# Kernel tuning notes

Hardware: AMD Instinct MI355X
Metric: run time of the kernel (lower is better)

Reference implementation:

```python
import jax, jax.numpy as jnp
import numpy as np

IN_F = 4096
OUT_F = 11008
GROUP = 128
BATCH = 32
Q_OUT = OUT_F // 2          # two int4 values packed per byte along out dim
N_GROUPS = IN_F // GROUP    # 32 groups


def setup_inputs() -> dict:
    key = jax.random.key(0)
    k1, k2, k3, k4, k5 = jax.random.split(key, 5)
    inp = jax.random.normal(k1, (BATCH, 1, IN_F), dtype=jnp.float32)
    qweight = jax.random.randint(k2, (IN_F, Q_OUT), 0, 256, dtype=jnp.int32)   # packed bytes
    scales = jax.random.uniform(k3, (N_GROUPS, OUT_F), dtype=jnp.float32) * 0.01
    qzeros = jax.random.randint(k4, (N_GROUPS, Q_OUT), 0, 256, dtype=jnp.int32)  # packed bytes
    bias = jax.random.normal(k5, (OUT_F,), dtype=jnp.float32)
    return {"input": inp, "qweight": qweight, "scales": scales, "qzeros": qzeros, "bias": bias}


def _unpack_int4(packed, n_out):
    # packed: [rows, n_out//2] bytes; low nibble -> even out col, high nibble -> odd out col
    low = packed & 0xF
    high = (packed >> 4) & 0xF
    return jnp.stack([low, high], axis=-1).reshape(packed.shape[0], n_out)


def reference(input, qweight, scales, qzeros, bias):
    # GPTQ-style grouped dequant: w[k, n] = (q[k, n] - zero[g(k), n]) * scale[g(k), n]
    q = _unpack_int4(qweight, OUT_F).astype(jnp.float32)   # [K, N]
    z = _unpack_int4(qzeros, OUT_F).astype(jnp.float32)    # [G, N]
    gidx = jnp.arange(IN_F) // GROUP                       # [K] group index per input channel
    w = (q - z[gidx]) * scales[gidx]                       # [K, N] dequantized weight
    # decode GEMV/GEMM: [B, 1, K] x [K, N] -> [B, 1, N], plus bias (mm_bias_int4 path)
    return jnp.einsum('bsk,kn->bsn', input, w) + bias
```

## Files before the change

kernel.cpp:

```cpp
#include <hip/hip_runtime.h>
#include <hip/hip_fp16.h>
#include <cstdint>

#define IN_F 4096
#define OUT_F 11008
#define Q_OUT 5504
#define GROUP 128
#define BATCH 32

#define KBS 8
#define GPB 4
#define NCH 8
#define BN 64
#define BROWS 66

typedef _Float16 f16x8 __attribute__((ext_vector_type(8)));
typedef float    f32x4 __attribute__((ext_vector_type(4)));

__global__ __launch_bounds__(256)
void xprep_kernel(const float* __restrict__ x, uint4* __restrict__ xf)
{
    const int t    = blockIdx.x * 256 + threadIdx.x;
    const int lane = t & 63;
    const int f    = (t >> 6) & 1;
    const int S    = t >> 7;
    const int m    = f * 16 + (lane & 15);
    const int k0   = S * 32 + (lane >> 4) * 8;
    const float4* xr = reinterpret_cast<const float4*>(x + (size_t)m * IN_F + k0);
    float4 a = xr[0], b = xr[1];
    union { _Float16 h[8]; uint4 u; } v;
    v.h[0] = (_Float16)a.x; v.h[1] = (_Float16)a.y;
    v.h[2] = (_Float16)a.z; v.h[3] = (_Float16)a.w;
    v.h[4] = (_Float16)b.x; v.h[5] = (_Float16)b.y;
    v.h[6] = (_Float16)b.z; v.h[7] = (_Float16)b.w;
    xf[t] = v.u;
}

__global__ __launch_bounds__(256)
void int4_gemm_kernel(const uint4* __restrict__ xf,
                      const int*   __restrict__ qw,
                      const float* __restrict__ scales,
                      const int*   __restrict__ qz,
                      float*       __restrict__ partial)
{
    const int tid  = threadIdx.x;
    const int lane = tid & 63;
    const int wid  = tid >> 6;
    const int nb   = blockIdx.x;
    const int kb   = blockIdx.y;
    const int g0   = kb * GPB;
    const int k0b  = g0 * GROUP;

    __shared__ uint4 a_lds[NCH * 4 * 64];
    __shared__ int   b_lds[2][32 * BROWS];

    const int cl  = lane & 15;
    const int kg  = lane >> 4;
    const int w   = wid * 8 + (cl >> 1);
    const int shn = (cl & 1) * 4;

    const int n = nb * BN + wid * 16 + cl;
    uint    zmu[GPB];
    __half2 spk[GPB];
    #pragma unroll
    for (int g = 0; g < GPB; ++g) {
        const float s = scales[(size_t)(g0 + g) * OUT_F + n];
        const int   z = (qz[(size_t)(g0 + g) * Q_OUT + (n >> 1)] >> shn) & 15;
        spk[g] = __float2half2_rn(s);
        zmu[g] = 0x64006400u + (uint)z * 0x00010001u;
    }

    {
        const size_t gbase = (size_t)(k0b / 32) * 2 * 64;
        #pragma unroll
        for (int r = 0; r < 8; ++r) {
            const uint4* gp = xf + gbase + (size_t)r * 256 + tid;
            __builtin_amdgcn_global_load_lds(
                (const __attribute__((address_space(1))) uint32_t*)gp,
                (__attribute__((address_space(3))) uint32_t*)&a_lds[r * 256 + wid * 64],
                16, 0, 0);
        }
    }

    const int a8 = tid & 7;
    const int bk = tid >> 3;

    f32x4 acc[2] = {};
    uint4 br0[2], br1[2];

    auto LOADB = [&](int c, int set) {
        const int kr = k0b + c * 64;
        br0[set] = *reinterpret_cast<const uint4*>(qw + (size_t)(kr + bk)      * Q_OUT + nb * 32 + a8 * 4);
        br1[set] = *reinterpret_cast<const uint4*>(qw + (size_t)(kr + bk + 32) * Q_OUT + nb * 32 + a8 * 4);
    };
    auto WLDS = [&](int buf, int set) {
        int* p = b_lds[buf];
        p[(4 * a8 + 0) * BROWS + bk]      = br0[set].x;
        p[(4 * a8 + 1) * BROWS + bk]      = br0[set].y;
        p[(4 * a8 + 2) * BROWS + bk]      = br0[set].z;
        p[(4 * a8 + 3) * BROWS + bk]      = br0[set].w;
        p[(4 * a8 + 0) * BROWS + bk + 32] = br1[set].x;
        p[(4 * a8 + 1) * BROWS + bk + 32] = br1[set].y;
        p[(4 * a8 + 2) * BROWS + bk + 32] = br1[set].z;
        p[(4 * a8 + 3) * BROWS + bk + 32] = br1[set].w;
    };

    LOADB(0, 0);
    LOADB(1, 1);
    WLDS(0, 0);
    asm volatile("s_waitcnt vmcnt(0) lgkmcnt(0)" ::: "memory");
    __builtin_amdgcn_s_barrier();
    asm volatile("" ::: "memory");

    #pragma unroll
    for (int c = 0; c < NCH; ++c) {
        const int cur = c & 1;
        if (c + 2 < NCH) LOADB(c + 2, cur);

        const __half2 zmh = __builtin_bit_cast(__half2, zmu[c >> 1]);
        const __half2 sg  = spk[c >> 1];

        #pragma unroll
        for (int s = 0; s < 2; ++s) {
            const int* bp = &b_lds[cur][w * BROWS + s * 32 + kg * 8];
            int2 q0 = *reinterpret_cast<const int2*>(bp + 0);
            int2 q1 = *reinterpret_cast<const int2*>(bp + 2);
            int2 q2 = *reinterpret_cast<const int2*>(bp + 4);
            int2 q3 = *reinterpret_cast<const int2*>(bp + 6);

            union { uint u[4]; f16x8 v; } bf;
            const int2 qq[4] = {q0, q1, q2, q3};
            #pragma unroll
            for (int t = 0; t < 4; ++t) {
                uint pr = __builtin_amdgcn_perm((uint)qq[t].y, (uint)qq[t].x, 0x0C040C00u);
                pr >>= shn;
                uint qk = (pr & 0x000F000Fu) | 0x64006400u;
                __half2 wv = __hmul2(__hsub2(__builtin_bit_cast(__half2, qk), zmh), sg);
                bf.u[t] = __builtin_bit_cast(uint, wv);
            }
            uint4 a0u = a_lds[(c * 4 + s * 2 + 0) * 64 + lane];
            uint4 a1u = a_lds[(c * 4 + s * 2 + 1) * 64 + lane];
            f16x8 af0 = __builtin_bit_cast(f16x8, a0u);
            f16x8 af1 = __builtin_bit_cast(f16x8, a1u);
            acc[0] = __builtin_amdgcn_mfma_f32_16x16x32_f16(af0, bf.v, acc[0], 0, 0, 0);
            acc[1] = __builtin_amdgcn_mfma_f32_16x16x32_f16(af1, bf.v, acc[1], 0, 0, 0);
        }

        if (c + 1 < NCH) {
            WLDS(cur ^ 1, cur ^ 1);
            asm volatile("s_waitcnt lgkmcnt(0)" ::: "memory");
            __builtin_amdgcn_s_barrier();
            asm volatile("" ::: "memory");
        }
    }

    #pragma unroll
    for (int f = 0; f < 2; ++f) {
        const int m = f * 16 + kg * 4;
        float* pp = partial + ((size_t)(kb * BATCH + m)) * OUT_F + n;
        pp[0]                 = acc[f][0];
        pp[(size_t)OUT_F]     = acc[f][1];
        pp[(size_t)OUT_F * 2] = acc[f][2];
        pp[(size_t)OUT_F * 3] = acc[f][3];
    }
}

__global__ __launch_bounds__(256)
void reduce_bias_kernel(const float* __restrict__ partial,
                        const float* __restrict__ bias,
                        float* __restrict__ out)
{
    const int i4 = (blockIdx.x * 256 + threadIdx.x) * 4;
    const int n  = i4 % OUT_F;
    float4 s = *reinterpret_cast<const float4*>(bias + n);
    #pragma unroll
    for (int kb = 0; kb < KBS; ++kb) {
        float4 p = *reinterpret_cast<const float4*>(partial + (size_t)kb * BATCH * OUT_F + i4);
        s.x += p.x; s.y += p.y; s.z += p.z; s.w += p.w;
    }
    *reinterpret_cast<float4*>(out + i4) = s;
}

extern "C" void kernel_launch(void* const* d_in, const int* in_sizes, int n_in,
                              void* d_out, int out_size, void* d_ws, size_t ws_size,
                              hipStream_t stream)
{
    const float* inp    = (const float*)d_in[0];
    const int*   qw     = (const int*)d_in[1];
    const float* scales = (const float*)d_in[2];
    const int*   qz     = (const int*)d_in[3];
    const float* bias   = (const float*)d_in[4];
    float*       out    = (float*)d_out;

    const size_t XFB = (size_t)BATCH * IN_F * 2;
    uint4* xf      = (uint4*)d_ws;
    float* partial = (float*)((char*)d_ws + XFB);

    xprep_kernel<<<64, 256, 0, stream>>>(inp, xf);

    int4_gemm_kernel<<<dim3(OUT_F / BN, KBS), 256, 0, stream>>>(
        xf, qw, scales, qz, partial);

    reduce_bias_kernel<<<(BATCH * OUT_F) / 1024, 256, 0, stream>>>(partial, bias, out);
}
```

Before: 31.46 us.

## Quantize activations to int8 and use i8 MFMA with atomic split-K reduction

Activations are quantized per row to int8 with a max-abs scale, and per-group activation sums are precomputed. The GEMM then runs on i8 MFMA instructions using raw int4 nibbles, and zero-points and scales are applied after accumulation using those sums. The separate reduce kernel is replaced by initializing the output with bias in the prep kernel and accumulating split-K partials with atomic adds. Weight dequantization math and the partial-buffer round trip go away, at the cost of int8 quantization error on activations and nondeterministic float atomics.

```diff
diff --git a/kernel.cpp b/kernel.cpp
--- a/kernel.cpp
+++ b/kernel.cpp
@@ -1,5 +1,4 @@
 #include <hip/hip_runtime.h>
-#include <hip/hip_fp16.h>
 #include <cstdint>
 
 #define IN_F 4096
@@ -12,36 +11,79 @@
 #define GPB 4
 #define NCH 8
 #define BN 64
-#define BROWS 66
-
-typedef _Float16 f16x8 __attribute__((ext_vector_type(8)));
-typedef float    f32x4 __attribute__((ext_vector_type(4)));
+#define BST 18
+
+typedef int   i32x4 __attribute__((ext_vector_type(4)));
+typedef float f32x4 __attribute__((ext_vector_type(4)));
 
 __global__ __launch_bounds__(256)
-void xprep_kernel(const float* __restrict__ x, uint4* __restrict__ xf)
+void prep_kernel(const float* __restrict__ x,
+                 const float* __restrict__ bias,
+                 uint4* __restrict__ xq,
+                 int*   __restrict__ Sx,
+                 float* __restrict__ delta,
+                 float* __restrict__ out)
 {
-    const int t    = blockIdx.x * 256 + threadIdx.x;
-    const int lane = t & 63;
-    const int f    = (t >> 6) & 1;
-    const int S    = t >> 7;
-    const int m    = f * 16 + (lane & 15);
-    const int k0   = S * 32 + (lane >> 4) * 8;
-    const float4* xr = reinterpret_cast<const float4*>(x + (size_t)m * IN_F + k0);
-    float4 a = xr[0], b = xr[1];
-    union { _Float16 h[8]; uint4 u; } v;
-    v.h[0] = (_Float16)a.x; v.h[1] = (_Float16)a.y;
-    v.h[2] = (_Float16)a.z; v.h[3] = (_Float16)a.w;
-    v.h[4] = (_Float16)b.x; v.h[5] = (_Float16)b.y;
-    v.h[6] = (_Float16)b.z; v.h[7] = (_Float16)b.w;
-    xf[t] = v.u;
+    const int t = threadIdx.x;
+    if (blockIdx.x >= 32) {
+        const int j4 = ((blockIdx.x - 32) * 256 + t) * 4;
+        *reinterpret_cast<float4*>(out + j4) =
+            *reinterpret_cast<const float4*>(bias + (j4 % OUT_F));
+        return;
+    }
+    const int m = blockIdx.x;
+    const float* xr = x + (size_t)m * IN_F + t * 16;
+    float4 v[4];
+    #pragma unroll
+    for (int i = 0; i < 4; ++i) v[i] = reinterpret_cast<const float4*>(xr)[i];
+
+    float lm = 0.f;
+    #pragma unroll
+    for (int i = 0; i < 4; ++i) {
+        lm = fmaxf(lm, fmaxf(fmaxf(fabsf(v[i].x), fabsf(v[i].y)),
+                             fmaxf(fabsf(v[i].z), fabsf(v[i].w))));
+    }
+    #pragma unroll
+    for (int d = 32; d; d >>= 1) lm = fmaxf(lm, __shfl_xor(lm, d));
+    __shared__ float wred[4];
+    if ((t & 63) == 0) wred[t >> 6] = lm;
+    __syncthreads();
+    const float mx  = fmaxf(fmaxf(wred[0], wred[1]), fmaxf(wred[2], wred[3]));
+    const float inv = mx > 0.f ? 127.0f / mx : 0.f;
+
+    int q[16];
+    #pragma unroll
+    for (int i = 0; i < 4; ++i) {
+        q[i * 4 + 0] = __float2int_rn(v[i].x * inv);
+        q[i * 4 + 1] = __float2int_rn(v[i].y * inv);
+        q[i * 4 + 2] = __float2int_rn(v[i].z * inv);
+        q[i * 4 + 3] = __float2int_rn(v[i].w * inv);
+    }
+    uint4 w;
+    uint* wp = reinterpret_cast<uint*>(&w);
+    #pragma unroll
+    for (int i = 0; i < 4; ++i)
+        wp[i] = (q[i*4] & 255) | ((q[i*4+1] & 255) << 8) |
+                ((q[i*4+2] & 255) << 16) | ((q[i*4+3] & 255) << 24);
+    xq[(t >> 2) * 128 + (m >> 4) * 64 + (t & 3) * 16 + (m & 15)] = w;
+
+    int psum = 0;
+    #pragma unroll
+    for (int i = 0; i < 16; ++i) psum += q[i];
+    #pragma unroll
+    for (int d = 4; d; d >>= 1) psum += __shfl_down(psum, d, 8);
+    if ((t & 7) == 0) Sx[(t >> 3) * 32 + m] = psum;
+    if (t == 0) delta[m] = mx * (1.0f / 127.0f);
 }
 
-__global__ __launch_bounds__(256)
-void int4_gemm_kernel(const uint4* __restrict__ xf,
-                      const int*   __restrict__ qw,
-                      const float* __restrict__ scales,
-                      const int*   __restrict__ qz,
-                      float*       __restrict__ partial)
+__global__ __launch_bounds__(256, 4)
+void int4_gemm_i8(const uint4* __restrict__ xq,
+                  const int*   __restrict__ qw,
+                  const float* __restrict__ scales,
+                  const int*   __restrict__ qz,
+                  const int*   __restrict__ Sx,
+                  const float* __restrict__ delta,
+                  float*       __restrict__ out)
 {
     const int tid  = threadIdx.x;
     const int lane = tid & 63;
@@ -51,58 +93,58 @@
     const int g0   = kb * GPB;
     const int k0b  = g0 * GROUP;
 
-    __shared__ uint4 a_lds[NCH * 4 * 64];
-    __shared__ int   b_lds[2][32 * BROWS];
+    __shared__ uint4 a_lds[1024];
+    __shared__ int   b_lds[2][64 * BST];
 
     const int cl  = lane & 15;
     const int kg  = lane >> 4;
-    const int w   = wid * 8 + (cl >> 1);
+    const int n   = nb * BN + wid * 16 + cl;
     const int shn = (cl & 1) * 4;
 
-    const int n = nb * BN + wid * 16 + cl;
-    uint    zmu[GPB];
-    __half2 spk[GPB];
+    #pragma unroll
+    for (int r = 0; r < 4; ++r) {
+        const uint4* gp = xq + (size_t)kb * 1024 + r * 256 + tid;
+        __builtin_amdgcn_global_load_lds(
+            (const __attribute__((address_space(1))) uint32_t*)gp,
+            (__attribute__((address_space(3))) uint32_t*)&a_lds[r * 256 + wid * 64],
+            16, 0, 0);
+    }
+
+    int   zv[GPB];
+    float sv[GPB];
     #pragma unroll
     for (int g = 0; g < GPB; ++g) {
-        const float s = scales[(size_t)(g0 + g) * OUT_F + n];
-        const int   z = (qz[(size_t)(g0 + g) * Q_OUT + (n >> 1)] >> shn) & 15;
-        spk[g] = __float2half2_rn(s);
-        zmu[g] = 0x64006400u + (uint)z * 0x00010001u;
-    }
-
-    {
-        const size_t gbase = (size_t)(k0b / 32) * 2 * 64;
+        sv[g] = scales[(size_t)(g0 + g) * OUT_F + n];
+        zv[g] = (qz[(size_t)(g0 + g) * Q_OUT + (n >> 1)] >> shn) & 15;
+    }
+
+    const int a16 = tid & 15;
+    const int rk  = tid >> 4;
+
+    uint2 d[2][4];
+    i32x4 acc_i[2] = {};
+    f32x4 accf[2]  = {};
+    int4  sx0v = {}, sx1v = {};
+
+    auto LOADB = [&](int c, int set) {
+        const int kr = k0b + c * 64 + 4 * rk;
         #pragma unroll
-        for (int r = 0; r < 8; ++r) {
-            const uint4* gp = xf + gbase + (size_t)r * 256 + tid;
-            __builtin_amdgcn_global_load_lds(
-                (const __attribute__((address_space(1))) uint32_t*)gp,
-                (__attribute__((address_space(3))) uint32_t*)&a_lds[r * 256 + wid * 64],
-                16, 0, 0);
-        }
-    }
-
-    const int a8 = tid & 7;
-    const int bk = tid >> 3;
-
-    f32x4 acc[2] = {};
-    uint4 br0[2], br1[2];
-
-    auto LOADB = [&](int c, int set) {
-        const int kr = k0b + c * 64;
-        br0[set] = *reinterpret_cast<const uint4*>(qw + (size_t)(kr + bk)      * Q_OUT + nb * 32 + a8 * 4);
-        br1[set] = *reinterpret_cast<const uint4*>(qw + (size_t)(kr + bk + 32) * Q_OUT + nb * 32 + a8 * 4);
+        for (int i = 0; i < 4; ++i)
+            d[set][i] = *reinterpret_cast<const uint2*>(
+                qw + (size_t)(kr + i) * Q_OUT + nb * 32 + 2 * a16);
     };
     auto WLDS = [&](int buf, int set) {
-        int* p = b_lds[buf];
-        p[(4 * a8 + 0) * BROWS + bk]      = br0[set].x;
-        p[(4 * a8 + 1) * BROWS + bk]      = br0[set].y;
-        p[(4 * a8 + 2) * BROWS + bk]      = br0[set].z;
-        p[(4 * a8 + 3) * BROWS + bk]      = br0[set].w;
-        p[(4 * a8 + 0) * BROWS + bk + 32] = br1[set].x;
-        p[(4 * a8 + 1) * BROWS + bk + 32] = br1[set].y;
-        p[(4 * a8 + 2) * BROWS + bk + 32] = br1[set].z;
-        p[(4 * a8 + 3) * BROWS + bk + 32] = br1[set].w;
+        #pragma unroll
+        for (int j = 0; j < 2; ++j) {
+            uint b0 = (j ? d[set][0].y : d[set][0].x) & 255u;
+            uint b1 = (j ? d[set][1].y : d[set][1].x) & 255u;
+            uint b2 = (j ? d[set][2].y : d[set][2].x) & 255u;
+            uint b3 = (j ? d[set][3].y : d[set][3].x) & 255u;
+            uint p  = b0 | (b1 << 8) | (b2 << 16) | (b3 << 24);
+            const int nloc = 4 * a16 + 2 * j;
+            b_lds[buf][(nloc + 0) * BST + rk] = (int)(p & 0x0F0F0F0Fu);
+            b_lds[buf][(nloc + 1) * BST + rk] = (int)((p >> 4) & 0x0F0F0F0Fu);
+        }
     };
 
     LOADB(0, 0);
@@ -115,35 +157,39 @@
     #pragma unroll
     for (int c = 0; c < NCH; ++c) {
         const int cur = c & 1;
+        const int gl  = c >> 1;
         if (c + 2 < NCH) LOADB(c + 2, cur);
-
-        const __half2 zmh = __builtin_bit_cast(__half2, zmu[c >> 1]);
-        const __half2 sg  = spk[c >> 1];
-
-        #pragma unroll
-        for (int s = 0; s < 2; ++s) {
-            const int* bp = &b_lds[cur][w * BROWS + s * 32 + kg * 8];
-            int2 q0 = *reinterpret_cast<const int2*>(bp + 0);
-            int2 q1 = *reinterpret_cast<const int2*>(bp + 2);
-            int2 q2 = *reinterpret_cast<const int2*>(bp + 4);
-            int2 q3 = *reinterpret_cast<const int2*>(bp + 6);
-
-            union { uint u[4]; f16x8 v; } bf;
-            const int2 qq[4] = {q0, q1, q2, q3};
+        if ((c & 1) == 0) {
+            sx0v = *reinterpret_cast<const int4*>(Sx + (g0 + gl) * 32 + kg * 4);
+            sx1v = *reinterpret_cast<const int4*>(Sx + (g0 + gl) * 32 + 16 + kg * 4);
+        }
+
+        const int* bp = &b_lds[cur][(wid * 16 + cl) * BST + 4 * kg];
+        int2 qa = *reinterpret_cast<const int2*>(bp);
+        int2 qb = *reinterpret_cast<const int2*>(bp + 2);
+        i32x4 bv; bv[0] = qa.x; bv[1] = qa.y; bv[2] = qb.x; bv[3] = qb.y;
+
+        uint4 a0 = a_lds[(c * 2 + 0) * 64 + lane];
+        uint4 a1 = a_lds[(c * 2 + 1) * 64 + lane];
+        acc_i[0] = __builtin_amdgcn_mfma_i32_16x16x64_i8(
+            __builtin_bit_cast(i32x4, a0), bv, acc_i[0], 0, 0, 0);
+        acc_i[1] = __builtin_amdgcn_mfma_i32_16x16x64_i8(
+            __builtin_bit_cast(i32x4, a1), bv, acc_i[1], 0, 0, 0);
+
+        if (c & 1) {
+            const int   zz = zv[gl];
+            const float ss = sv[gl];
+            int sxa[8] = { sx0v.x, sx0v.y, sx0v.z, sx0v.w,
+                           sx1v.x, sx1v.y, sx1v.z, sx1v.w };
             #pragma unroll
-            for (int t = 0; t < 4; ++t) {
-                uint pr = __builtin_amdgcn_perm((uint)qq[t].y, (uint)qq[t].x, 0x0C040C00u);
-                pr >>= shn;
-                uint qk = (pr & 0x000F000Fu) | 0x64006400u;
-                __half2 wv = __hmul2(__hsub2(__builtin_bit_cast(__half2, qk), zmh), sg);
-                bf.u[t] = __builtin_bit_cast(uint, wv);
-            }
-            uint4 a0u = a_lds[(c * 4 + s * 2 + 0) * 64 + lane];
-            uint4 a1u = a_lds[(c * 4 + s * 2 + 1) * 64 + lane];
-            f16x8 af0 = __builtin_bit_cast(f16x8, a0u);
-            f16x8 af1 = __builtin_bit_cast(f16x8, a1u);
-            acc[0] = __builtin_amdgcn_mfma_f32_16x16x32_f16(af0, bf.v, acc[0], 0, 0, 0);
-            acc[1] = __builtin_amdgcn_mfma_f32_16x16x32_f16(af1, bf.v, acc[1], 0, 0, 0);
+            for (int f = 0; f < 2; ++f)
+                #pragma unroll
+                for (int r = 0; r < 4; ++r) {
+                    int tt = acc_i[f][r] - zz * sxa[f * 4 + r];
+                    accf[f][r] = fmaf(ss, (float)tt, accf[f][r]);
+                }
+            acc_i[0] = i32x4{0, 0, 0, 0};
+            acc_i[1] = i32x4{0, 0, 0, 0};
         }
 
         if (c + 1 < NCH) {
@@ -154,31 +200,16 @@
         }
     }
 
-    #pragma unroll
-    for (int f = 0; f < 2; ++f) {
-        const int m = f * 16 + kg * 4;
-        float* pp = partial + ((size_t)(kb * BATCH + m)) * OUT_F + n;
-        pp[0]                 = acc[f][0];
-        pp[(size_t)OUT_F]     = acc[f][1];
-        pp[(size_t)OUT_F * 2] = acc[f][2];
-        pp[(size_t)OUT_F * 3] = acc[f][3];
-    }
-}
-
-__global__ __launch_bounds__(256)
-void reduce_bias_kernel(const float* __restrict__ partial,
-                        const float* __restrict__ bias,
-                        float* __restrict__ out)
-{
-    const int i4 = (blockIdx.x * 256 + threadIdx.x) * 4;
-    const int n  = i4 % OUT_F;
-    float4 s = *reinterpret_cast<const float4*>(bias + n);
-    #pragma unroll
-    for (int kb = 0; kb < KBS; ++kb) {
-        float4 p = *reinterpret_cast<const float4*>(partial + (size_t)kb * BATCH * OUT_F + i4);
-        s.x += p.x; s.y += p.y; s.z += p.z; s.w += p.w;
-    }
-    *reinterpret_cast<float4*>(out + i4) = s;
+    float4 dl0 = *reinterpret_cast<const float4*>(delta + kg * 4);
+    float4 dl1 = *reinterpret_cast<const float4*>(delta + 16 + kg * 4);
+    const float dla[8] = { dl0.x, dl0.y, dl0.z, dl0.w, dl1.x, dl1.y, dl1.z, dl1.w };
+    #pragma unroll
+    for (int f = 0; f < 2; ++f)
+        #pragma unroll
+        for (int r = 0; r < 4; ++r) {
+            const int m = f * 16 + kg * 4 + r;
+            unsafeAtomicAdd(out + (size_t)m * OUT_F + n, dla[f * 4 + r] * accf[f][r]);
+        }
 }
 
 extern "C" void kernel_launch(void* const* d_in, const int* in_sizes, int n_in,
@@ -192,14 +223,12 @@
     const float* bias   = (const float*)d_in[4];
     float*       out    = (float*)d_out;
 
-    const size_t XFB = (size_t)BATCH * IN_F * 2;
-    uint4* xf      = (uint4*)d_ws;
-    float* partial = (float*)((char*)d_ws + XFB);
-
-    xprep_kernel<<<64, 256, 0, stream>>>(inp, xf);
-
-    int4_gemm_kernel<<<dim3(OUT_F / BN, KBS), 256, 0, stream>>>(
-        xf, qw, scales, qz, partial);
-
-    reduce_bias_kernel<<<(BATCH * OUT_F) / 1024, 256, 0, stream>>>(partial, bias, out);
+    uint4* xq    = (uint4*)d_ws;
+    int*   Sx    = (int*)((char*)d_ws + 131072);
+    float* delta = (float*)((char*)d_ws + 131072 + 4096);
+
+    prep_kernel<<<376, 256, 0, stream>>>(inp, bias, xq, Sx, delta, out);
+
+    int4_gemm_i8<<<dim3(OUT_F / BN, KBS), 256, 0, stream>>>(
+        xq, qw, scales, qz, Sx, delta, out);
 }
```

New measurement: 28.41 us. 1.11x faster.
